# Kernel optimization log

Hardware: AMD Instinct MI355X
Metric: run time of the kernel (lower is better)

Reference implementation:

```python
import jax, jax.numpy as jnp
import numpy as np

T = 16384
G = 8
D_IN = 2048
D_OUT = 8192
# uneven per-expert group sizes summing exactly to T (torch.split requires this)
_GROUP_SIZES = np.array([1024, 3072, 2048, 512, 4096, 1536, 2560, 1536], dtype=np.int64)
assert _GROUP_SIZES.sum() == T


def setup_inputs() -> dict:
    key = jax.random.key(0)
    k_x, k_w = jax.random.split(key)
    hidden_states = jax.random.normal(k_x, (T, D_IN), dtype=jnp.float32)
    # kaiming_uniform_(a=sqrt(5)) on [G, out, in] -> bound = 1/sqrt(in_features)
    bound = 1.0 / np.sqrt(D_IN)
    weight = jax.random.uniform(k_w, (G, D_OUT, D_IN), dtype=jnp.float32,
                                minval=-bound, maxval=bound)
    offsets = jnp.asarray(np.cumsum(_GROUP_SIZES), dtype=jnp.int64)
    return {"hidden_states": hidden_states, "offsets": offsets, "weight": weight}


def reference(hidden_states, offsets, weight):
    # grouped GEMM: for group g, rows [offsets[g-1]:offsets[g]] @ weight[g].T
    # weight is [G, out, in]; torch transposes last two dims -> rhs [G, in, out]
    group_sizes = jnp.diff(offsets, prepend=jnp.zeros((1,), offsets.dtype)).astype(jnp.int32)
    rhs = jnp.swapaxes(weight, -1, -2)  # [G, in, out]
    return jax.lax.ragged_dot(hidden_states, rhs, group_sizes)  # [T, out]
```

## Files before the change

### kernel.cpp

```cpp
#include <hip/hip_runtime.h>
#include <stdint.h>

#define T_TOK   16384
#define D_INK   2048
#define D_OUTN  8192
#define G_NUM   8

#define BM 256
#define BN 256
#define BK 64
#define NKT (D_INK / BK)
#define MT_TILES (T_TOK / BM)
#define NT_TILES (D_OUTN / BN)

typedef __attribute__((ext_vector_type(8))) short bf16x8;
typedef __attribute__((ext_vector_type(4))) float f32x4;

#define BARRIER() do { asm volatile("" ::: "memory"); __builtin_amdgcn_s_barrier(); asm volatile("" ::: "memory"); } while (0)
#define VMCNT(n)  asm volatile("s_waitcnt vmcnt(" #n ")" ::: "memory")
#define MFMA16(d,vw,vx) d = __builtin_amdgcn_mfma_f32_16x16x32_bf16(vw, vx, d, 0, 0, 0)

__device__ __forceinline__ unsigned int f2bf(float f) {
    union { float f; unsigned int u; } v; v.f = f;
    unsigned int u = v.u;
    unsigned int r = u + 0x7FFFu + ((u >> 16) & 1u);
    return r >> 16;
}

__global__ __launch_bounds__(256) void cvt_f32_bf16(const float* __restrict__ src,
                                                    unsigned short* __restrict__ dst,
                                                    long long n8) {
    long long i = (long long)blockIdx.x * blockDim.x + threadIdx.x;
    long long stride = (long long)gridDim.x * blockDim.x;
    const float4* s4 = reinterpret_cast<const float4*>(src);
    for (; i < n8; i += stride) {
        float4 x = s4[i * 2];
        float4 y = s4[i * 2 + 1];
        uint4 o;
        o.x = f2bf(x.x) | (f2bf(x.y) << 16);
        o.y = f2bf(x.z) | (f2bf(x.w) << 16);
        o.z = f2bf(y.x) | (f2bf(y.y) << 16);
        o.w = f2bf(y.z) | (f2bf(y.w) << 16);
        *reinterpret_cast<uint4*>(dst + i * 8) = o;
    }
}

__device__ __forceinline__ void gload_lds16(const unsigned short* g, void* l) {
    __builtin_amdgcn_global_load_lds(
        (const __attribute__((address_space(1))) void*)g,
        (__attribute__((address_space(3))) void*)l,
        16, 0, 0);
}

__global__ __launch_bounds__(512, 2) void grouped_gemm_256(
    const unsigned short* __restrict__ Abf,
    const unsigned short* __restrict__ Wbf,
    const int* __restrict__ offs_raw,
    float* __restrict__ out)
{
    __shared__ unsigned short lds[2][32768];

    const int tid  = threadIdx.x;
    const int wave = tid >> 6;
    const int lane = tid & 63;

    const int swz = (blockIdx.x & 7) * (MT_TILES * NT_TILES / 8) + (blockIdx.x >> 3);
    const int set = swz >> 5;
    const int idx = swz & 31;
    const int nt = (set & 7) * 4 + (idx & 3);
    const int mt = (set >> 3) * 8 + (idx >> 2);

    const int row0 = mt * BM;
    const int col0 = nt * BN;

    const int ostride = (offs_raw[1] == 0) ? 2 : 1;
    int g = 0;
#pragma unroll
    for (int i = 0; i < G_NUM - 1; ++i)
        if (row0 >= offs_raw[i * ostride]) g = i + 1;

    const unsigned short* Aorig = Abf + (size_t)row0 * D_INK;
    const unsigned short* Worig = Wbf + ((size_t)g * D_OUTN + col0) * D_INK;

    const int lrow = lane >> 2;
    const int gcol_off = ((lane & 3) * 8) ^ ((lane & 32) ? 16 : 0);

    const int fr  = lane & 15;
    const int fk2 = (lane >> 4) << 4;
    const int swz_off = fr * 64 + (fk2 ^ ((fr & 8) ? 32 : 0));
    const int wm16 = (wave >> 2) * 8;
    const int wn16 = (wave & 3) * 4;
    const int wm = (wave >> 2) * 128;
    const int wn = (wave & 3) * 64;

    char* ldsc = (char*)&lds[0][0];

    auto stageAh = [&](int buf, int kt, int h) {
#pragma unroll
        for (int i = 0; i < 2; ++i) {
            const int s = h * 16 + i * 8 + wave;
            const int sr = s >> 1, sc = s & 1;
            const unsigned short* src = Aorig + (size_t)(sr * 16 + lrow) * D_INK
                                        + kt * BK + sc * 32 + gcol_off;
            gload_lds16(src, ldsc + buf * 65536 + s * 1024);
        }
    };
    auto stageBh = [&](int buf, int kt, int h) {
#pragma unroll
        for (int i = 0; i < 2; ++i) {
            const int s = h * 16 + i * 8 + wave;
            const int sr = s >> 1, sc = s & 1;
            const unsigned short* src = Worig + (size_t)(sr * 16 + lrow) * D_INK
                                        + kt * BK + sc * 32 + gcol_off;
            gload_lds16(src, ldsc + buf * 65536 + 32768 + s * 1024);
        }
    };

    f32x4 acc[8][4] = {};
    bf16x8 a[4][2], b[4][2];

    auto ldB2 = [&](int buf, int jb) {
#pragma unroll
        for (int j = 0; j < 2; ++j) {
            const int sr = wn16 + jb + j;
            b[jb + j][0] = *reinterpret_cast<const bf16x8*>(ldsc + buf * 65536 + 32768 + (sr * 2 + 0) * 1024 + swz_off);
            b[jb + j][1] = *reinterpret_cast<const bf16x8*>(ldsc + buf * 65536 + 32768 + (sr * 2 + 1) * 1024 + swz_off);
        }
    };
    auto ldA4 = [&](int buf, int mb) {
#pragma unroll
        for (int i = 0; i < 4; ++i) {
            const int sr = wm16 + mb + i;
            a[i][0] = *reinterpret_cast<const bf16x8*>(ldsc + buf * 65536 + (sr * 2 + 0) * 1024 + swz_off);
            a[i][1] = *reinterpret_cast<const bf16x8*>(ldsc + buf * 65536 + (sr * 2 + 1) * 1024 + swz_off);
        }
    };
    auto quad = [&](int ib, int jb) {
        __builtin_amdgcn_s_setprio(1);
#pragma unroll
        for (int i = 0; i < 4; ++i)
#pragma unroll
            for (int j = 0; j < 2; ++j) {
                MFMA16(acc[ib + i][jb + j], b[jb + j][0], a[i][0]);
                MFMA16(acc[ib + i][jb + j], b[jb + j][1], a[i][1]);
            }
        __builtin_amdgcn_s_setprio(0);
    };

    stageBh(0, 0, 0); stageBh(0, 0, 1);
    stageAh(0, 0, 0); stageAh(0, 0, 1);
    stageBh(1, 1, 0); stageBh(1, 1, 1);
    VMCNT(4);
    BARRIER();

    for (int t = 0; t < NKT; t += 2) {
        const bool s2 = (t + 2 < NKT), s3 = (t + 3 < NKT);

        ldB2(0, 0); ldA4(0, 0);
        stageAh(1, t + 1, 0);
        BARRIER(); quad(0, 0); BARRIER();

        ldB2(0, 2);
        stageAh(1, t + 1, 1);
        BARRIER(); quad(0, 2); BARRIER();

        ldA4(0, 4);
        if (s2) stageBh(0, t + 2, 0);
        BARRIER(); quad(4, 0); BARRIER();

        if (s2) stageBh(0, t + 2, 1);
        BARRIER();
        quad(4, 2);
        if (s2) { VMCNT(4); } else { VMCNT(0); }
        BARRIER();

        ldB2(1, 0); ldA4(1, 0);
        if (s2) stageAh(0, t + 2, 0);
        BARRIER(); quad(0, 0); BARRIER();

        ldB2(1, 2);
        if (s2) stageAh(0, t + 2, 1);
        BARRIER(); quad(0, 2); BARRIER();

        ldA4(1, 4);
        if (s3) stageBh(1, t + 3, 0);
        BARRIER(); quad(4, 0); BARRIER();

        if (s3) stageBh(1, t + 3, 1);
        BARRIER();
        quad(4, 2);
        if (s3) { VMCNT(4); } else { VMCNT(0); }
        BARRIER();
    }

    const int m_in   = lane & 15;
    const int n_base = (lane >> 4) * 4;
#pragma unroll
    for (int i = 0; i < 8; ++i) {
        const size_t rbase = (size_t)(row0 + wm + i * 16 + m_in) * D_OUTN;
#pragma unroll
        for (int j = 0; j < 4; ++j) {
            const int cc = col0 + wn + j * 16 + n_base;
            *reinterpret_cast<f32x4*>(&out[rbase + cc]) = acc[i][j];
        }
    }
}

__global__ __launch_bounds__(256) void naive_grouped(
    const float* __restrict__ A, const float* __restrict__ W,
    const int* __restrict__ offs_raw, float* __restrict__ out)
{
    const long long total = (long long)T_TOK * D_OUTN;
    long long idx = (long long)blockIdx.x * blockDim.x + threadIdx.x;
    const long long stride = (long long)gridDim.x * blockDim.x;
    const int ostride = (offs_raw[1] == 0) ? 2 : 1;
    for (; idx < total; idx += stride) {
        const int t = (int)(idx / D_OUTN);
        const int c = (int)(idx % D_OUTN);
        int g = 0;
        for (int i = 0; i < G_NUM - 1; ++i)
            if (t >= offs_raw[i * ostride]) g = i + 1;
        const float4* a4 = reinterpret_cast<const float4*>(A + (size_t)t * D_INK);
        const float4* w4 = reinterpret_cast<const float4*>(W + ((size_t)g * D_OUTN + c) * D_INK);
        float s = 0.f;
        for (int k = 0; k < D_INK / 4; ++k) {
            float4 av = a4[k], wv = w4[k];
            s += av.x * wv.x + av.y * wv.y + av.z * wv.z + av.w * wv.w;
        }
        out[idx] = s;
    }
}

extern "C" void kernel_launch(void* const* d_in, const int* in_sizes, int n_in,
                              void* d_out, int out_size, void* d_ws, size_t ws_size,
                              hipStream_t stream) {
    const float* hidden = (const float*)d_in[0];
    const int*   offs   = (const int*)d_in[1];
    const float* weight = (const float*)d_in[2];
    float* out = (float*)d_out;

    const size_t nA = (size_t)T_TOK * D_INK;
    const size_t nW = (size_t)G_NUM * D_OUTN * D_INK;
    const size_t need = (nA + nW) * sizeof(unsigned short);

    if (ws_size >= need) {
        unsigned short* Abf = (unsigned short*)d_ws;
        unsigned short* Wbf = Abf + nA;
        cvt_f32_bf16<<<2048, 256, 0, stream>>>(hidden, Abf, (long long)(nA / 8));
        cvt_f32_bf16<<<4096, 256, 0, stream>>>(weight, Wbf, (long long)(nW / 8));
        grouped_gemm_256<<<MT_TILES * NT_TILES, 512, 0, stream>>>(Abf, Wbf, offs, out);
    } else {
        naive_grouped<<<8192, 256, 0, stream>>>(hidden, weight, offs, out);
    }
}
```

Before: 724.5 us.

## Make grouped GEMM persistent and overlap next tile prologue with epilogue stores

```diff
diff --git a/kernel.cpp b/kernel.cpp
--- a/kernel.cpp
+++ b/kernel.cpp
@@ -12,12 +12,14 @@
 #define NKT (D_INK / BK)
 #define MT_TILES (T_TOK / BM)
 #define NT_TILES (D_OUTN / BN)
+#define TILES_PER_BLK 8
 
 typedef __attribute__((ext_vector_type(8))) short bf16x8;
 typedef __attribute__((ext_vector_type(4))) float f32x4;
 
 #define BARRIER() do { asm volatile("" ::: "memory"); __builtin_amdgcn_s_barrier(); asm volatile("" ::: "memory"); } while (0)
 #define VMCNT(n)  asm volatile("s_waitcnt vmcnt(" #n ")" ::: "memory")
+#define CFENCE()  asm volatile("" ::: "memory")
 #define MFMA16(d,vw,vx) d = __builtin_amdgcn_mfma_f32_16x16x32_bf16(vw, vx, d, 0, 0, 0)
 
 __device__ __forceinline__ unsigned int f2bf(float f) {
@@ -64,23 +66,7 @@
     const int wave = tid >> 6;
     const int lane = tid & 63;
 
-    const int swz = (blockIdx.x & 7) * (MT_TILES * NT_TILES / 8) + (blockIdx.x >> 3);
-    const int set = swz >> 5;
-    const int idx = swz & 31;
-    const int nt = (set & 7) * 4 + (idx & 3);
-    const int mt = (set >> 3) * 8 + (idx >> 2);
-
-    const int row0 = mt * BM;
-    const int col0 = nt * BN;
-
     const int ostride = (offs_raw[1] == 0) ? 2 : 1;
-    int g = 0;
-#pragma unroll
-    for (int i = 0; i < G_NUM - 1; ++i)
-        if (row0 >= offs_raw[i * ostride]) g = i + 1;
-
-    const unsigned short* Aorig = Abf + (size_t)row0 * D_INK;
-    const unsigned short* Worig = Wbf + ((size_t)g * D_OUTN + col0) * D_INK;
 
     const int lrow = lane >> 2;
     const int gcol_off = ((lane & 3) * 8) ^ ((lane & 32) ? 16 : 0);
@@ -95,6 +81,27 @@
 
     char* ldsc = (char*)&lds[0][0];
 
+    int row0 = 0, col0 = 0;
+    const unsigned short* Aorig = Abf;
+    const unsigned short* Worig = Wbf;
+
+    auto setTile = [&](int it) {
+        const int seq = it * 256 + blockIdx.x;
+        const int swz = (seq & 7) * (MT_TILES * NT_TILES / 8) + (seq >> 3);
+        const int set = swz >> 5;
+        const int idx = swz & 31;
+        const int nt = (set & 7) * 4 + (idx & 3);
+        const int mt = (set >> 3) * 8 + (idx >> 2);
+        row0 = mt * BM;
+        col0 = nt * BN;
+        int g = 0;
+#pragma unroll
+        for (int i = 0; i < G_NUM - 1; ++i)
+            if (row0 >= offs_raw[i * ostride]) g = i + 1;
+        Aorig = Abf + (size_t)row0 * D_INK;
+        Worig = Wbf + ((size_t)g * D_OUTN + col0) * D_INK;
+    };
+
     auto stageAh = [&](int buf, int kt, int h) {
 #pragma unroll
         for (int i = 0; i < 2; ++i) {
@@ -115,6 +122,11 @@
             gload_lds16(src, ldsc + buf * 65536 + 32768 + s * 1024);
         }
     };
+    auto prologue = [&]() {
+        stageBh(0, 0, 0); stageBh(0, 0, 1);
+        stageAh(0, 0, 0); stageAh(0, 0, 1);
+        stageBh(1, 1, 0); stageBh(1, 1, 1);
+    };
 
     f32x4 acc[8][4] = {};
     bf16x8 a[4][2], b[4][2];
@@ -147,61 +159,83 @@
         __builtin_amdgcn_s_setprio(0);
     };
 
-    stageBh(0, 0, 0); stageBh(0, 0, 1);
-    stageAh(0, 0, 0); stageAh(0, 0, 1);
-    stageBh(1, 1, 0); stageBh(1, 1, 1);
+    setTile(0);
+    prologue();
     VMCNT(4);
     BARRIER();
 
-    for (int t = 0; t < NKT; t += 2) {
-        const bool s2 = (t + 2 < NKT), s3 = (t + 3 < NKT);
-
-        ldB2(0, 0); ldA4(0, 0);
-        stageAh(1, t + 1, 0);
-        BARRIER(); quad(0, 0); BARRIER();
-
-        ldB2(0, 2);
-        stageAh(1, t + 1, 1);
-        BARRIER(); quad(0, 2); BARRIER();
-
-        ldA4(0, 4);
-        if (s2) stageBh(0, t + 2, 0);
-        BARRIER(); quad(4, 0); BARRIER();
-
-        if (s2) stageBh(0, t + 2, 1);
-        BARRIER();
-        quad(4, 2);
-        if (s2) { VMCNT(4); } else { VMCNT(0); }
-        BARRIER();
-
-        ldB2(1, 0); ldA4(1, 0);
-        if (s2) stageAh(0, t + 2, 0);
-        BARRIER(); quad(0, 0); BARRIER();
-
-        ldB2(1, 2);
-        if (s2) stageAh(0, t + 2, 1);
-        BARRIER(); quad(0, 2); BARRIER();
-
-        ldA4(1, 4);
-        if (s3) stageBh(1, t + 3, 0);
-        BARRIER(); quad(4, 0); BARRIER();
-
-        if (s3) stageBh(1, t + 3, 1);
-        BARRIER();
-        quad(4, 2);
-        if (s3) { VMCNT(4); } else { VMCNT(0); }
-        BARRIER();
-    }
-
-    const int m_in   = lane & 15;
-    const int n_base = (lane >> 4) * 4;
-#pragma unroll
-    for (int i = 0; i < 8; ++i) {
-        const size_t rbase = (size_t)(row0 + wm + i * 16 + m_in) * D_OUTN;
-#pragma unroll
-        for (int j = 0; j < 4; ++j) {
-            const int cc = col0 + wn + j * 16 + n_base;
-            *reinterpret_cast<f32x4*>(&out[rbase + cc]) = acc[i][j];
+#pragma unroll 1
+    for (int it = 0; it < TILES_PER_BLK; ++it) {
+
+        for (int t = 0; t < NKT; t += 2) {
+            const bool s2 = (t + 2 < NKT), s3 = (t + 3 < NKT);
+
+            ldB2(0, 0); ldA4(0, 0);
+            stageAh(1, t + 1, 0);
+            BARRIER(); quad(0, 0); BARRIER();
+
+            ldB2(0, 2);
+            stageAh(1, t + 1, 1);
+            BARRIER(); quad(0, 2); BARRIER();
+
+            ldA4(0, 4);
+            if (s2) stageBh(0, t + 2, 0);
+            BARRIER(); quad(4, 0); BARRIER();
+
+            if (s2) stageBh(0, t + 2, 1);
+            BARRIER();
+            quad(4, 2);
+            if (s2) { VMCNT(4); } else { VMCNT(0); }
+            BARRIER();
+
+            ldB2(1, 0); ldA4(1, 0);
+            if (s2) stageAh(0, t + 2, 0);
+            BARRIER(); quad(0, 0); BARRIER();
+
+            ldB2(1, 2);
+            if (s2) stageAh(0, t + 2, 1);
+            BARRIER(); quad(0, 2); BARRIER();
+
+            ldA4(1, 4);
+            if (s3) stageBh(1, t + 3, 0);
+            BARRIER(); quad(4, 0); BARRIER();
+
+            if (s3) stageBh(1, t + 3, 1);
+            BARRIER();
+            quad(4, 2);
+            if (s3) { VMCNT(4); } else { VMCNT(0); }
+            BARRIER();
+        }
+
+        const int srow0 = row0, scol0 = col0;
+
+        if (it + 1 < TILES_PER_BLK) {
+            setTile(it + 1);
+            prologue();
+            CFENCE();
+        }
+
+        const int m_in   = lane & 15;
+        const int n_base = (lane >> 4) * 4;
+#pragma unroll
+        for (int i = 0; i < 8; ++i) {
+            const size_t rbase = (size_t)(srow0 + wm + i * 16 + m_in) * D_OUTN;
+#pragma unroll
+            for (int j = 0; j < 4; ++j) {
+                const int cc = scol0 + wn + j * 16 + n_base;
+                *reinterpret_cast<f32x4*>(&out[rbase + cc]) = acc[i][j];
+            }
+        }
+
+        if (it + 1 < TILES_PER_BLK) {
+#pragma unroll
+            for (int i = 0; i < 8; ++i)
+#pragma unroll
+                for (int j = 0; j < 4; ++j)
+#pragma unroll
+                    for (int r = 0; r < 4; ++r) acc[i][j][r] = 0.0f;
+            VMCNT(36);
+            BARRIER();
         }
     }
 }
@@ -248,7 +282,7 @@
         unsigned short* Wbf = Abf + nA;
         cvt_f32_bf16<<<2048, 256, 0, stream>>>(hidden, Abf, (long long)(nA / 8));
         cvt_f32_bf16<<<4096, 256, 0, stream>>>(weight, Wbf, (long long)(nW / 8));
-        grouped_gemm_256<<<MT_TILES * NT_TILES, 512, 0, stream>>>(Abf, Wbf, offs, out);
+        grouped_gemm_256<<<256, 512, 0, stream>>>(Abf, Wbf, offs, out);
     } else {
         naive_grouped<<<8192, 256, 0, stream>>>(hidden, weight, offs, out);
     }
```

New measurement: 755.8 us. 1.04x slower.

## Split MFMA inner loop by k-half and remap tile order to M-chunks

Applied to the files above, without the earlier changes.

```diff
diff --git a/kernel.cpp b/kernel.cpp
--- a/kernel.cpp
+++ b/kernel.cpp
@@ -12,6 +12,7 @@
 #define NKT (D_INK / BK)
 #define MT_TILES (T_TOK / BM)
 #define NT_TILES (D_OUTN / BN)
+#define MCHUNK 4
 
 typedef __attribute__((ext_vector_type(8))) short bf16x8;
 typedef __attribute__((ext_vector_type(4))) float f32x4;
@@ -65,10 +66,11 @@
     const int lane = tid & 63;
 
     const int swz = (blockIdx.x & 7) * (MT_TILES * NT_TILES / 8) + (blockIdx.x >> 3);
-    const int set = swz >> 5;
-    const int idx = swz & 31;
-    const int nt = (set & 7) * 4 + (idx & 3);
-    const int mt = (set >> 3) * 8 + (idx >> 2);
+    const int per_chunk = MCHUNK * NT_TILES;
+    const int chunk = swz / per_chunk;
+    const int rem   = swz % per_chunk;
+    const int nt = rem >> 2;
+    const int mt = chunk * MCHUNK + (rem & (MCHUNK - 1));
 
     const int row0 = mt * BM;
     const int col0 = nt * BN;
@@ -117,33 +119,27 @@
     };
 
     f32x4 acc[8][4] = {};
-    bf16x8 a[4][2], b[4][2];
-
-    auto ldB2 = [&](int buf, int jb) {
-#pragma unroll
-        for (int j = 0; j < 2; ++j) {
-            const int sr = wn16 + jb + j;
-            b[jb + j][0] = *reinterpret_cast<const bf16x8*>(ldsc + buf * 65536 + 32768 + (sr * 2 + 0) * 1024 + swz_off);
-            b[jb + j][1] = *reinterpret_cast<const bf16x8*>(ldsc + buf * 65536 + 32768 + (sr * 2 + 1) * 1024 + swz_off);
-        }
-    };
-    auto ldA4 = [&](int buf, int mb) {
-#pragma unroll
-        for (int i = 0; i < 4; ++i) {
-            const int sr = wm16 + mb + i;
-            a[i][0] = *reinterpret_cast<const bf16x8*>(ldsc + buf * 65536 + (sr * 2 + 0) * 1024 + swz_off);
-            a[i][1] = *reinterpret_cast<const bf16x8*>(ldsc + buf * 65536 + (sr * 2 + 1) * 1024 + swz_off);
-        }
-    };
-    auto quad = [&](int ib, int jb) {
+    bf16x8 a[4], a2[4], b[4];
+
+    auto ldB4 = [&](int buf, int ks) {
+#pragma unroll
+        for (int j = 0; j < 4; ++j)
+            b[j] = *reinterpret_cast<const bf16x8*>(
+                ldsc + buf * 65536 + 32768 + ((wn16 + j) * 2 + ks) * 1024 + swz_off);
+    };
+    auto ldA4k = [&](int buf, int mb, int ks, bf16x8* dst) {
+#pragma unroll
+        for (int i = 0; i < 4; ++i)
+            dst[i] = *reinterpret_cast<const bf16x8*>(
+                ldsc + buf * 65536 + ((wm16 + mb + i) * 2 + ks) * 1024 + swz_off);
+    };
+    auto quad16 = [&](int ib, const bf16x8* av) {
         __builtin_amdgcn_s_setprio(1);
 #pragma unroll
         for (int i = 0; i < 4; ++i)
 #pragma unroll
-            for (int j = 0; j < 2; ++j) {
-                MFMA16(acc[ib + i][jb + j], b[jb + j][0], a[i][0]);
-                MFMA16(acc[ib + i][jb + j], b[jb + j][1], a[i][1]);
-            }
+            for (int j = 0; j < 4; ++j)
+                MFMA16(acc[ib + i][j], b[j], av[i]);
         __builtin_amdgcn_s_setprio(0);
     };
 
@@ -156,39 +152,41 @@
     for (int t = 0; t < NKT; t += 2) {
         const bool s2 = (t + 2 < NKT), s3 = (t + 3 < NKT);
 
-        ldB2(0, 0); ldA4(0, 0);
+        ldB4(0, 0); ldA4k(0, 0, 0, a);
         stageAh(1, t + 1, 0);
-        BARRIER(); quad(0, 0); BARRIER();
-
-        ldB2(0, 2);
+        BARRIER(); quad16(0, a); BARRIER();
+
+        ldA4k(0, 4, 0, a2);
         stageAh(1, t + 1, 1);
-        BARRIER(); quad(0, 2); BARRIER();
-
-        ldA4(0, 4);
+        BARRIER(); quad16(4, a2); BARRIER();
+
+        ldB4(0, 1); ldA4k(0, 0, 1, a);
         if (s2) stageBh(0, t + 2, 0);
-        BARRIER(); quad(4, 0); BARRIER();
-
+        BARRIER(); quad16(0, a); BARRIER();
+
+        ldA4k(0, 4, 1, a2);
         if (s2) stageBh(0, t + 2, 1);
         BARRIER();
-        quad(4, 2);
+        quad16(4, a2);
         if (s2) { VMCNT(4); } else { VMCNT(0); }
         BARRIER();
 
-        ldB2(1, 0); ldA4(1, 0);
+        ldB4(1, 0); ldA4k(1, 0, 0, a);
         if (s2) stageAh(0, t + 2, 0);
-        BARRIER(); quad(0, 0); BARRIER();
-
-        ldB2(1, 2);
+        BARRIER(); quad16(0, a); BARRIER();
+
+        ldA4k(1, 4, 0, a2);
         if (s2) stageAh(0, t + 2, 1);
-        BARRIER(); quad(0, 2); BARRIER();
-
-        ldA4(1, 4);
+        BARRIER(); quad16(4, a2); BARRIER();
+
+        ldB4(1, 1); ldA4k(1, 0, 1, a);
         if (s3) stageBh(1, t + 3, 0);
-        BARRIER(); quad(4, 0); BARRIER();
-
+        BARRIER(); quad16(0, a); BARRIER();
+
+        ldA4k(1, 4, 1, a2);
         if (s3) stageBh(1, t + 3, 1);
         BARRIER();
-        quad(4, 2);
+        quad16(4, a2);
         if (s3) { VMCNT(4); } else { VMCNT(0); }
         BARRIER();
     }
```

Result: slower. 1.182 ms (+63.2%).
